# Optimization experiments

Hardware: AMD Instinct MI355X
Metric: run time of the kernel (lower is better)

Reference implementation:

```python
import jax, jax.numpy as jnp
import numpy as np

EPS = 1e-5

def _proj(x, W, g, b, m, v):
    # 1x1 conv (no bias) + BatchNorm2d (inference stats) + ReLU
    y = jnp.einsum('bchw,oc->bohw', x, W)
    scale = g / jnp.sqrt(v + EPS)
    y = y * scale[:, None, None] + (b - m * scale)[:, None, None]
    return jax.nn.relu(y)

def setup_inputs() -> dict:
    key = jax.random.key(0)
    B, C, H, W = 4, 192, 64, 64
    ks = jax.random.split(key, 10)
    d = {
        'lr_hsi': jax.random.normal(ks[0], (B, C, H, W), jnp.float32),
        'refine_hsi': jax.random.normal(ks[1], (B, C, H, W), jnp.float32),
    }
    for i, name in enumerate(['q', 'k', 'v', 't']):
        d['W' + name] = jax.random.normal(ks[2 + i], (C, C), jnp.float32) * 0.05
        d['g' + name] = jnp.ones((C,), jnp.float32)
        d['b' + name] = jnp.zeros((C,), jnp.float32)
        d['m' + name] = jnp.zeros((C,), jnp.float32)
        d['v' + name] = jnp.ones((C,), jnp.float32)
    return d

def reference(lr_hsi, refine_hsi,
              Wq, gq, bq, mq, vq,
              Wk, gk, bk, mk, vk,
              Wv, gv, bv, mv, vv,
              Wt, gt, bt, mt, vt):
    B, C, H, W = refine_hsi.shape
    HW = H * W
    q = _proj(refine_hsi, Wq, gq, bq, mq, vq).reshape(B, C, HW).transpose(0, 2, 1)  # [B, HWq, C]
    k = _proj(lr_hsi, Wk, gk, bk, mk, vk).reshape(B, C, HW)                          # [B, C, HWk]
    v = _proj(lr_hsi, Wv, gv, bv, mv, vv).reshape(B, C, HW).transpose(0, 2, 1)      # [B, HWk, C]
    corr = jnp.einsum('bqc,bck->bqk', q, k) * (C ** -0.5)  # [B, HWq, HWk]
    corr = jax.nn.softmax(corr, axis=1)  # NOTE: softmax over the QUERY axis (dim=1), as in source
    ss = jnp.einsum('bqk,bkc->bqc', corr, v)               # [B, HWq, C]
    ss = ss.transpose(0, 2, 1).reshape(B, C, H, W)
    out = _proj(ss, Wt, gt, bt, mt, vt)
    return (out, corr)
```

## Files before the change

### kernel.cpp

```cpp
#include <hip/hip_runtime.h>
#include <math.h>

typedef __attribute__((ext_vector_type(4))) float f32x4;
typedef __attribute__((ext_vector_type(8))) short bf16x8;

__device__ __forceinline__ unsigned short f2bf(float f) {
  unsigned int u = __builtin_bit_cast(unsigned int, f);
  u += 0x7FFFu + ((u >> 16) & 1u);
  return (unsigned short)(u >> 16);
}

__device__ __forceinline__ f32x4 mfma16(bf16x8 a, bf16x8 b, f32x4 c) {
  return __builtin_amdgcn_mfma_f32_16x16x32_bf16(a, b, c, 0, 0, 0);
}

__global__ void prep_kernel(const float* __restrict__ W, const float* __restrict__ g,
                            const float* __restrict__ bb, const float* __restrict__ mm,
                            const float* __restrict__ vv,
                            unsigned short* __restrict__ Wout, float* __restrict__ bout,
                            float alpha) {
  int idx = blockIdx.x * 256 + threadIdx.x;
  if (idx < 192 * 192) {
    int o = idx / 192;
    float s = g[o] * rsqrtf(vv[o] + 1e-5f);
    Wout[idx] = f2bf(W[idx] * s * alpha);
  }
  if (idx < 192) {
    float s = g[idx] * rsqrtf(vv[idx] + 1e-5f);
    bout[idx] = (bb[idx] - mm[idx] * s) * alpha;
  }
}

template <int LAYOUT>
__launch_bounds__(256)
__global__ void proj_kernel(const float* __restrict__ X,
                            const unsigned short* __restrict__ Wp,
                            const float* __restrict__ bias,
                            unsigned short* __restrict__ Yv) {
  const int o0 = blockIdx.x * 64;
  const int hw0 = blockIdx.y * 64;
  const int b = blockIdx.z;
  const int w = threadIdx.x >> 6, l = threadIdx.x & 63;
  const int l16 = l & 15, lg = l >> 4;
  const float* Xb = X + (size_t)b * 192 * 4096;

  f32x4 acc[4] = {f32x4{0,0,0,0}, f32x4{0,0,0,0}, f32x4{0,0,0,0}, f32x4{0,0,0,0}};

  for (int ks = 0; ks < 6; ++ks) {
    const int c0 = ks * 32 + lg * 8;
    bf16x8 a = *(const bf16x8*)(Wp + (size_t)(o0 + 16 * w + l16) * 192 + c0);
#pragma unroll
    for (int n = 0; n < 4; ++n) {
      const int hw = hw0 + 16 * n + l16;
      bf16x8 bfr;
#pragma unroll
      for (int j = 0; j < 8; ++j)
        bfr[j] = (short)f2bf(Xb[(size_t)(c0 + j) * 4096 + hw]);
      acc[n] = mfma16(a, bfr, acc[n]);
    }
  }

#pragma unroll
  for (int n = 0; n < 4; ++n) {
    const int hw = hw0 + 16 * n + l16;
    float vv4[4];
#pragma unroll
    for (int r = 0; r < 4; ++r) {
      const int o = o0 + 16 * w + lg * 4 + r;
      vv4[r] = fmaxf(acc[n][r] + bias[o], 0.0f);
    }
    if (LAYOUT == 1) {
      unsigned int lo = (unsigned)f2bf(vv4[0]) | ((unsigned)f2bf(vv4[1]) << 16);
      unsigned int hi = (unsigned)f2bf(vv4[2]) | ((unsigned)f2bf(vv4[3]) << 16);
      uint2 pk; pk.x = lo; pk.y = hi;
      *(uint2*)(Yv + ((size_t)b * 4096 + hw) * 192 + o0 + 16 * w + lg * 4) = pk;
    } else {
#pragma unroll
      for (int r = 0; r < 4; ++r) {
        const int o = o0 + 16 * w + lg * 4 + r;
        Yv[((size_t)b * 192 + o) * 4096 + hw] = f2bf(vv4[r]);
      }
    }
  }
}

template <int NS>
__launch_bounds__(256)
__global__ void proj_sum_kernel(const float* __restrict__ X,
                                const unsigned short* __restrict__ Wp,
                                const float* __restrict__ bias,
                                float* __restrict__ Yv) {
  const int o0 = blockIdx.x * 64;
  const int hw0 = blockIdx.y * 64;
  const int b = blockIdx.z;
  const int w = threadIdx.x >> 6, l = threadIdx.x & 63;
  const int l16 = l & 15, lg = l >> 4;
  const float* Xb = X + (size_t)b * 192 * 4096;
  const size_t sstride = (size_t)4 * 192 * 4096;

  f32x4 acc[4] = {f32x4{0,0,0,0}, f32x4{0,0,0,0}, f32x4{0,0,0,0}, f32x4{0,0,0,0}};

  for (int ks = 0; ks < 6; ++ks) {
    const int c0 = ks * 32 + lg * 8;
    bf16x8 a = *(const bf16x8*)(Wp + (size_t)(o0 + 16 * w + l16) * 192 + c0);
#pragma unroll
    for (int n = 0; n < 4; ++n) {
      const int hw = hw0 + 16 * n + l16;
      bf16x8 bfr;
#pragma unroll
      for (int j = 0; j < 8; ++j) {
        float s = Xb[(size_t)(c0 + j) * 4096 + hw];
#pragma unroll
        for (int ss = 1; ss < NS; ++ss)
          s += Xb[(size_t)(c0 + j) * 4096 + hw + ss * sstride];
        bfr[j] = (short)f2bf(s);
      }
      acc[n] = mfma16(a, bfr, acc[n]);
    }
  }

#pragma unroll
  for (int n = 0; n < 4; ++n) {
    const int hw = hw0 + 16 * n + l16;
#pragma unroll
    for (int r = 0; r < 4; ++r) {
      const int o = o0 + 16 * w + lg * 4 + r;
      Yv[((size_t)b * 192 + o) * 4096 + hw] = fmaxf(acc[n][r] + bias[o], 0.0f);
    }
  }
}

__launch_bounds__(256)
__global__ void pass1_kernel(const unsigned short* __restrict__ qp,
                             const unsigned short* __restrict__ kpT,
                             float* __restrict__ colsum) {
  const int q0 = blockIdx.x * 128, k0 = blockIdx.y * 128, b = blockIdx.z;
  const int w = threadIdx.x >> 6, l = threadIdx.x & 63;
  const int l16 = l & 15, lg = l >> 4;
  const unsigned short* qb = qp + (size_t)b * 4096 * 192;
  const unsigned short* kb = kpT + (size_t)b * 4096 * 192;

  __shared__ __align__(16) unsigned short kpl[128][200];
  __shared__ float cs[4][128];

  {
    const int t = threadIdx.x;
#pragma unroll
    for (int i = 0; i < 12; ++i) {
      int idx = t + i * 256;
      int row = idx / 24, cu = idx % 24;
      uint4 vdat = *(const uint4*)(kb + (size_t)(k0 + row) * 192 + cu * 8);
      *(uint4*)&kpl[row][cu * 8] = vdat;
    }
  }
  __syncthreads();

  f32x4 acc[2][8];
#pragma unroll
  for (int m = 0; m < 2; ++m)
#pragma unroll
    for (int n = 0; n < 8; ++n) acc[m][n] = f32x4{0, 0, 0, 0};

  for (int ks = 0; ks < 6; ++ks) {
    const int c0 = ks * 32 + lg * 8;
    bf16x8 a0 = *(const bf16x8*)(qb + (size_t)(q0 + 32 * w + l16) * 192 + c0);
    bf16x8 a1 = *(const bf16x8*)(qb + (size_t)(q0 + 32 * w + 16 + l16) * 192 + c0);
#pragma unroll
    for (int n = 0; n < 8; ++n) {
      bf16x8 bfr = *(const bf16x8*)&kpl[16 * n + l16][c0];
      acc[0][n] = mfma16(a0, bfr, acc[0][n]);
      acc[1][n] = mfma16(a1, bfr, acc[1][n]);
    }
  }

  float part[8];
#pragma unroll
  for (int n = 0; n < 8; ++n) {
    float s = 0.f;
#pragma unroll
    for (int r = 0; r < 4; ++r)
      s += __builtin_amdgcn_exp2f(acc[0][n][r]) + __builtin_amdgcn_exp2f(acc[1][n][r]);
    s += __shfl_xor(s, 16);
    s += __shfl_xor(s, 32);
    part[n] = s;
  }
  if (l < 16) {
#pragma unroll
    for (int n = 0; n < 8; ++n) cs[w][16 * n + l] = part[n];
  }
  __syncthreads();
  const int t = threadIdx.x;
  if (t < 128) {
    float s = cs[0][t] + cs[1][t] + cs[2][t] + cs[3][t];
    atomicAdd(&colsum[(size_t)b * 4096 + k0 + t], s);
  }
}

__global__ void invert_kernel(float* __restrict__ p, int n) {
  int i = blockIdx.x * 256 + threadIdx.x;
  if (i < n) p[i] = 1.0f / p[i];
}

template <int NS>
__launch_bounds__(512)
__global__ void pass2_kernel(const unsigned short* __restrict__ qp,
                             const unsigned short* __restrict__ kpT,
                             const unsigned short* __restrict__ vpN,
                             const float* __restrict__ rcol,
                             float* __restrict__ corr,
                             float* __restrict__ ssP) {
  const int q0 = blockIdx.x * 64;
  const int s = blockIdx.y;
  const int b = blockIdx.z;
  const int kc0 = s * (32 / NS);
  const int w = threadIdx.x >> 6, l = threadIdx.x & 63;
  const int l16 = l & 15, lg = l >> 4;
  const int mw = w & 1, nw = w >> 1;
  const unsigned short* qb = qp + (size_t)b * 4096 * 192;
  const unsigned short* kb = kpT + (size_t)b * 4096 * 192;
  const unsigned short* vb = vpN + (size_t)b * 192 * 4096;
  const float* rc = rcol + (size_t)b * 4096;
  float* corb = corr + (size_t)b * 4096 * 4096;
  float* ssb = ssP + (size_t)(s * 4 + b) * 192 * 4096;

  __shared__ __align__(16) float cor[64][132];

  bf16x8 af[2][6];
#pragma unroll
  for (int tm = 0; tm < 2; ++tm)
#pragma unroll
    for (int ks = 0; ks < 6; ++ks)
      af[tm][ks] = *(const bf16x8*)(qb + (size_t)(q0 + 16 * (2 * mw + tm) + l16) * 192 + ks * 32 + lg * 8);

  f32x4 ssa[2][3];
#pragma unroll
  for (int tm = 0; tm < 2; ++tm)
#pragma unroll
    for (int j = 0; j < 3; ++j) ssa[tm][j] = f32x4{0, 0, 0, 0};

  for (int kc = kc0; kc < kc0 + 32 / NS; ++kc) {
    const int k0 = kc * 128;
    f32x4 sa[2][2];
#pragma unroll
    for (int tm = 0; tm < 2; ++tm)
#pragma unroll
      for (int tn = 0; tn < 2; ++tn) sa[tm][tn] = f32x4{0, 0, 0, 0};

    for (int ks = 0; ks < 6; ++ks) {
      const int c0 = ks * 32 + lg * 8;
#pragma unroll
      for (int tn = 0; tn < 2; ++tn) {
        const int kcol = k0 + 16 * (2 * nw + tn) + l16;
        bf16x8 bfr = *(const bf16x8*)(kb + (size_t)kcol * 192 + c0);
        sa[0][tn] = mfma16(af[0][ks], bfr, sa[0][tn]);
        sa[1][tn] = mfma16(af[1][ks], bfr, sa[1][tn]);
      }
    }
    float rcv[2];
#pragma unroll
    for (int tn = 0; tn < 2; ++tn) rcv[tn] = rc[k0 + 16 * (2 * nw + tn) + l16];
#pragma unroll
    for (int tm = 0; tm < 2; ++tm)
#pragma unroll
      for (int tn = 0; tn < 2; ++tn)
#pragma unroll
        for (int r = 0; r < 4; ++r)
          sa[tm][tn][r] = __builtin_amdgcn_exp2f(sa[tm][tn][r]) * rcv[tn];

    __syncthreads();
#pragma unroll
    for (int tm = 0; tm < 2; ++tm)
#pragma unroll
      for (int tn = 0; tn < 2; ++tn) {
        const int col = 16 * (2 * nw + tn) + l16;
#pragma unroll
        for (int r = 0; r < 4; ++r)
          cor[16 * (2 * mw + tm) + lg * 4 + r][col] = sa[tm][tn][r];
      }
    __syncthreads();

    {
      const int t = threadIdx.x;
#pragma unroll
      for (int it = 0; it < 4; ++it) {
        int idx = t + it * 512;
        int row = idx >> 5, seg = idx & 31;
        f32x4 v4 = *(const f32x4*)&cor[row][seg * 4];
        __builtin_nontemporal_store(v4, (f32x4*)(corb + (size_t)(q0 + row) * 4096 + k0 + seg * 4));
      }
    }

#pragma unroll
    for (int ks2 = 0; ks2 < 4; ++ks2) {
      const int cc = ks2 * 32 + lg * 8;
      bf16x8 pa[2];
#pragma unroll
      for (int tm = 0; tm < 2; ++tm) {
        f32x4 p0 = *(const f32x4*)&cor[16 * (2 * mw + tm) + l16][cc];
        f32x4 p1 = *(const f32x4*)&cor[16 * (2 * mw + tm) + l16][cc + 4];
#pragma unroll
        for (int j = 0; j < 4; ++j) {
          pa[tm][j] = (short)f2bf(p0[j]);
          pa[tm][j + 4] = (short)f2bf(p1[j]);
        }
      }
#pragma unroll
      for (int j = 0; j < 3; ++j) {
        const int ccol = 16 * (nw + 4 * j) + l16;
        bf16x8 bfr = *(const bf16x8*)(vb + (size_t)ccol * 4096 + k0 + cc);
        ssa[0][j] = mfma16(pa[0], bfr, ssa[0][j]);
        ssa[1][j] = mfma16(pa[1], bfr, ssa[1][j]);
      }
    }
  }

#pragma unroll
  for (int tm = 0; tm < 2; ++tm)
#pragma unroll
    for (int j = 0; j < 3; ++j) {
      const int ccol = 16 * (nw + 4 * j) + l16;
#pragma unroll
      for (int r = 0; r < 4; ++r) {
        const int qrow = q0 + 16 * (2 * mw + tm) + lg * 4 + r;
        ssb[(size_t)ccol * 4096 + qrow] = ssa[tm][j][r];
      }
    }
}

extern "C" void kernel_launch(void* const* d_in, const int* in_sizes, int n_in,
                              void* d_out, int out_size, void* d_ws, size_t ws_size,
                              hipStream_t stream) {
  (void)in_sizes; (void)n_in; (void)out_size;
  const float* lr = (const float*)d_in[0];
  const float* refine = (const float*)d_in[1];

  char* ws = (char*)d_ws;
  unsigned short* w4 = (unsigned short*)(ws + 0);
  float* bias4 = (float*)(ws + 294912);
  unsigned short* qp = (unsigned short*)(ws + 297984);
  unsigned short* kp = (unsigned short*)(ws + 297984 + 6291456);
  unsigned short* vp = (unsigned short*)(ws + 297984 + 2 * 6291456);
  float* colsum = (float*)(ws + 297984 + 3 * 6291456);
  float* ssP = (float*)(ws + 297984 + 3 * 6291456 + 65536);

  const size_t base = 297984 + (size_t)3 * 6291456 + 65536;
  const size_t slab = (size_t)4 * 192 * 4096 * 4;
  int NS = (ws_size >= base + 2 * slab) ? 2 : 1;

  float* out0 = (float*)d_out;
  float* corr = out0 + 3145728;

  const float alpha = (float)(1.4426950408889634 / sqrt(192.0));

  for (int p = 0; p < 4; ++p) {
    prep_kernel<<<dim3(144), dim3(256), 0, stream>>>(
        (const float*)d_in[2 + 5 * p], (const float*)d_in[3 + 5 * p],
        (const float*)d_in[4 + 5 * p], (const float*)d_in[5 + 5 * p],
        (const float*)d_in[6 + 5 * p],
        w4 + p * 36864, bias4 + p * 192, p == 0 ? alpha : 1.0f);
  }
  hipMemsetAsync(colsum, 0, 65536, stream);

  proj_kernel<1><<<dim3(3, 64, 4), dim3(256), 0, stream>>>(refine, w4, bias4, qp);
  proj_kernel<1><<<dim3(3, 64, 4), dim3(256), 0, stream>>>(lr, w4 + 36864, bias4 + 192, kp);
  proj_kernel<0><<<dim3(3, 64, 4), dim3(256), 0, stream>>>(lr, w4 + 2 * 36864, bias4 + 2 * 192, vp);

  pass1_kernel<<<dim3(32, 32, 4), dim3(256), 0, stream>>>(qp, kp, colsum);
  invert_kernel<<<dim3(64), dim3(256), 0, stream>>>(colsum, 16384);

  if (NS == 2) {
    pass2_kernel<2><<<dim3(64, 2, 4), dim3(512), 0, stream>>>(qp, kp, vp, colsum, corr, ssP);
    proj_sum_kernel<2><<<dim3(3, 64, 4), dim3(256), 0, stream>>>(ssP, w4 + 3 * 36864, bias4 + 3 * 192, out0);
  } else {
    pass2_kernel<1><<<dim3(64, 1, 4), dim3(512), 0, stream>>>(qp, kp, vp, colsum, corr, ssP);
    proj_sum_kernel<1><<<dim3(3, 64, 4), dim3(256), 0, stream>>>(ssP, w4 + 3 * 36864, bias4 + 3 * 192, out0);
  }
}
```

Before: 293.8 us.

## Stage K tiles in swizzled double-buffered LDS and shrink key chunk to 64

The pass2 kernel now loads each 64-key K tile cooperatively into a double-buffered, XOR-swizzled shared-memory buffer. The next tile is prefetched into registers during the current tile's MFMAs and written to LDS afterwards, replacing the per-wave direct global loads of K fragments. The key chunk shrinks from 128 to 64 columns, with a matching smaller correlation staging buffer and adjusted store and PV loops. Launch bounds now request 4 blocks per CU, which constrains register use; the added LDS (about 65 KB per block) may itself limit occupancy.

```diff
diff --git a/kernel.cpp b/kernel.cpp
--- a/kernel.cpp
+++ b/kernel.cpp
@@ -202,7 +202,7 @@
 }
 
 template <int NS>
-__launch_bounds__(512)
+__launch_bounds__(512, 4)
 __global__ void pass2_kernel(const unsigned short* __restrict__ qp,
                              const unsigned short* __restrict__ kpT,
                              const unsigned short* __restrict__ vpN,
@@ -212,7 +212,8 @@
   const int q0 = blockIdx.x * 64;
   const int s = blockIdx.y;
   const int b = blockIdx.z;
-  const int kc0 = s * (32 / NS);
+  const int nchunk = 64 / NS;
+  const int kc0 = s * nchunk;
   const int w = threadIdx.x >> 6, l = threadIdx.x & 63;
   const int l16 = l & 15, lg = l >> 4;
   const int mw = w & 1, nw = w >> 1;
@@ -223,7 +224,11 @@
   float* corb = corr + (size_t)b * 4096 * 4096;
   float* ssb = ssP + (size_t)(s * 4 + b) * 192 * 4096;
 
-  __shared__ __align__(16) float cor[64][132];
+  __shared__ __align__(16) unsigned short kst[2][64 * 192];
+  __shared__ __align__(16) float cor[64][66];
+
+  const int u0 = threadIdx.x;
+  const int srow = u0 / 24 >= 64 ? 63 : u0 / 24;
 
   bf16x8 af[2][6];
 #pragma unroll
@@ -238,60 +243,83 @@
 #pragma unroll
     for (int j = 0; j < 3; ++j) ssa[tm][j] = f32x4{0, 0, 0, 0};
 
-  for (int kc = kc0; kc < kc0 + 32 / NS; ++kc) {
-    const int k0 = kc * 128;
-    f32x4 sa[2][2];
-#pragma unroll
-    for (int tm = 0; tm < 2; ++tm)
-#pragma unroll
-      for (int tn = 0; tn < 2; ++tn) sa[tm][tn] = f32x4{0, 0, 0, 0};
-
+  {
+    const int k0 = kc0 * 64;
+#pragma unroll
+    for (int i = 0; i < 3; ++i) {
+      int u = u0 + i * 512;
+      int row = u / 24, cu = u % 24;
+      uint4 vdat = *(const uint4*)(kb + (size_t)(k0 + row) * 192 + cu * 8);
+      *(uint4*)&kst[0][row * 192 + ((cu * 8) ^ ((row & 7) << 3))] = vdat;
+    }
+  }
+  __syncthreads();
+
+  const int krow = 16 * nw + l16;
+  const int kswz = (krow & 7) << 3;
+
+  for (int kc = kc0; kc < kc0 + nchunk; ++kc) {
+    const int k0 = kc * 64;
+    const int cur = (kc - kc0) & 1;
+    const bool havenext = (kc + 1 < kc0 + nchunk);
+
+    uint4 stg[3];
+    if (havenext) {
+      const int k0n = k0 + 64;
+#pragma unroll
+      for (int i = 0; i < 3; ++i) {
+        int u = u0 + i * 512;
+        int row = u / 24, cu = u % 24;
+        stg[i] = *(const uint4*)(kb + (size_t)(k0n + row) * 192 + cu * 8);
+      }
+    }
+
+    f32x4 sa[2];
+    sa[0] = f32x4{0, 0, 0, 0};
+    sa[1] = f32x4{0, 0, 0, 0};
     for (int ks = 0; ks < 6; ++ks) {
       const int c0 = ks * 32 + lg * 8;
-#pragma unroll
-      for (int tn = 0; tn < 2; ++tn) {
-        const int kcol = k0 + 16 * (2 * nw + tn) + l16;
-        bf16x8 bfr = *(const bf16x8*)(kb + (size_t)kcol * 192 + c0);
-        sa[0][tn] = mfma16(af[0][ks], bfr, sa[0][tn]);
-        sa[1][tn] = mfma16(af[1][ks], bfr, sa[1][tn]);
-      }
-    }
-    float rcv[2];
-#pragma unroll
-    for (int tn = 0; tn < 2; ++tn) rcv[tn] = rc[k0 + 16 * (2 * nw + tn) + l16];
+      bf16x8 kf = *(const bf16x8*)&kst[cur][krow * 192 + (c0 ^ kswz)];
+      sa[0] = mfma16(af[0][ks], kf, sa[0]);
+      sa[1] = mfma16(af[1][ks], kf, sa[1]);
+    }
+    const float rcv = rc[k0 + krow];
 #pragma unroll
     for (int tm = 0; tm < 2; ++tm)
 #pragma unroll
-      for (int tn = 0; tn < 2; ++tn)
-#pragma unroll
-        for (int r = 0; r < 4; ++r)
-          sa[tm][tn][r] = __builtin_amdgcn_exp2f(sa[tm][tn][r]) * rcv[tn];
+      for (int r = 0; r < 4; ++r)
+        sa[tm][r] = __builtin_amdgcn_exp2f(sa[tm][r]) * rcv;
 
     __syncthreads();
-#pragma unroll
-    for (int tm = 0; tm < 2; ++tm)
-#pragma unroll
-      for (int tn = 0; tn < 2; ++tn) {
-        const int col = 16 * (2 * nw + tn) + l16;
-#pragma unroll
-        for (int r = 0; r < 4; ++r)
-          cor[16 * (2 * mw + tm) + lg * 4 + r][col] = sa[tm][tn][r];
-      }
+
+#pragma unroll
+    for (int tm = 0; tm < 2; ++tm) {
+#pragma unroll
+      for (int r = 0; r < 4; ++r)
+        cor[16 * (2 * mw + tm) + lg * 4 + r][krow] = sa[tm][r];
+    }
+    if (havenext) {
+#pragma unroll
+      for (int i = 0; i < 3; ++i) {
+        int u = u0 + i * 512;
+        int row = u / 24, cu = u % 24;
+        *(uint4*)&kst[cur ^ 1][row * 192 + ((cu * 8) ^ ((row & 7) << 3))] = stg[i];
+      }
+    }
     __syncthreads();
 
     {
-      const int t = threadIdx.x;
-#pragma unroll
-      for (int it = 0; it < 4; ++it) {
-        int idx = t + it * 512;
-        int row = idx >> 5, seg = idx & 31;
+#pragma unroll
+      for (int it = 0; it < 2; ++it) {
+        int u = u0 + it * 512;
+        int row = u >> 4, seg = u & 15;
         f32x4 v4 = *(const f32x4*)&cor[row][seg * 4];
         __builtin_nontemporal_store(v4, (f32x4*)(corb + (size_t)(q0 + row) * 4096 + k0 + seg * 4));
       }
     }
 
 #pragma unroll
-    for (int ks2 = 0; ks2 < 4; ++ks2) {
+    for (int ks2 = 0; ks2 < 2; ++ks2) {
       const int cc = ks2 * 32 + lg * 8;
       bf16x8 pa[2];
 #pragma unroll
```

Measured after the change: 334.2 us. +13.7%, slower.

## Materialize bf16 exp matrix once, fold column normalization into V, split PV and corr

Applied to the files above, without the earlier changes.

Pass 1 now stores the exponentiated scores as a bf16 E buffer alongside the column sums, so the QK^T product is no longer recomputed in pass 2. The softmax normalization moves into V through a scaled-V kernel, PV becomes a plain bf16 GEMM over E, and a separate streaming kernel writes corr from E times the reciprocal column sums. The cost is a 128MB intermediate write and read, plus bf16 rounding of the exponentials before both corr and the PV product. The new path runs only when the workspace is large enough, otherwise the old recompute path is used.

```diff
diff --git a/kernel.cpp b/kernel.cpp
--- a/kernel.cpp
+++ b/kernel.cpp
@@ -8,6 +8,10 @@
   unsigned int u = __builtin_bit_cast(unsigned int, f);
   u += 0x7FFFu + ((u >> 16) & 1u);
   return (unsigned short)(u >> 16);
+}
+
+__device__ __forceinline__ float bf2f(unsigned short u) {
+  return __builtin_bit_cast(float, (unsigned int)u << 16);
 }
 
 __device__ __forceinline__ f32x4 mfma16(bf16x8 a, bf16x8 b, f32x4 c) {
@@ -131,15 +135,200 @@
 }
 
 __launch_bounds__(256)
-__global__ void pass1_kernel(const unsigned short* __restrict__ qp,
-                             const unsigned short* __restrict__ kpT,
-                             float* __restrict__ colsum) {
+__global__ void pass1_e_kernel(const unsigned short* __restrict__ qp,
+                               const unsigned short* __restrict__ kpT,
+                               unsigned short* __restrict__ E,
+                               float* __restrict__ colsum) {
   const int q0 = blockIdx.x * 128, k0 = blockIdx.y * 128, b = blockIdx.z;
   const int w = threadIdx.x >> 6, l = threadIdx.x & 63;
   const int l16 = l & 15, lg = l >> 4;
   const unsigned short* qb = qp + (size_t)b * 4096 * 192;
   const unsigned short* kb = kpT + (size_t)b * 4096 * 192;
 
+  __shared__ __align__(16) unsigned short smem[128 * 200];
+
+  {
+    const int t = threadIdx.x;
+#pragma unroll
+    for (int i = 0; i < 12; ++i) {
+      int idx = t + i * 256;
+      int row = idx / 24, cu = idx % 24;
+      uint4 vdat = *(const uint4*)(qb + (size_t)(q0 + row) * 192 + cu * 8);
+      *(uint4*)&smem[row * 200 + cu * 8] = vdat;
+    }
+  }
+  __syncthreads();
+
+  f32x4 acc[2][8];
+#pragma unroll
+  for (int m = 0; m < 2; ++m)
+#pragma unroll
+    for (int n = 0; n < 8; ++n) acc[m][n] = f32x4{0, 0, 0, 0};
+
+  for (int ks = 0; ks < 6; ++ks) {
+    const int c0 = ks * 32 + lg * 8;
+    bf16x8 a0 = *(const bf16x8*)(kb + (size_t)(k0 + 32 * w + l16) * 192 + c0);
+    bf16x8 a1 = *(const bf16x8*)(kb + (size_t)(k0 + 32 * w + 16 + l16) * 192 + c0);
+#pragma unroll
+    for (int n = 0; n < 8; ++n) {
+      bf16x8 bfr = *(const bf16x8*)&smem[(16 * n + l16) * 200 + c0];
+      acc[0][n] = mfma16(a0, bfr, acc[0][n]);
+      acc[1][n] = mfma16(a1, bfr, acc[1][n]);
+    }
+  }
+
+#pragma unroll
+  for (int m = 0; m < 2; ++m) {
+#pragma unroll
+    for (int r = 0; r < 4; ++r) {
+      float s = 0.f;
+#pragma unroll
+      for (int n = 0; n < 8; ++n) {
+        float e = __builtin_amdgcn_exp2f(acc[m][n][r]);
+        acc[m][n][r] = e;
+        s += e;
+      }
+      s += __shfl_xor(s, 1);
+      s += __shfl_xor(s, 2);
+      s += __shfl_xor(s, 4);
+      s += __shfl_xor(s, 8);
+      if (l16 == 0)
+        atomicAdd(&colsum[(size_t)b * 4096 + k0 + 32 * w + 16 * m + lg * 4 + r], s);
+    }
+  }
+
+  __syncthreads();
+#pragma unroll
+  for (int m = 0; m < 2; ++m)
+#pragma unroll
+    for (int n = 0; n < 8; ++n) {
+      unsigned int lo = (unsigned)f2bf(acc[m][n][0]) | ((unsigned)f2bf(acc[m][n][1]) << 16);
+      unsigned int hi = (unsigned)f2bf(acc[m][n][2]) | ((unsigned)f2bf(acc[m][n][3]) << 16);
+      uint2 pk; pk.x = lo; pk.y = hi;
+      *(uint2*)&smem[(16 * n + l16) * 144 + 32 * w + 16 * m + lg * 4] = pk;
+    }
+  __syncthreads();
+
+  {
+    const int t = threadIdx.x;
+#pragma unroll
+    for (int i = 0; i < 8; ++i) {
+      int idx = t + i * 256;
+      int row = idx >> 4, c16 = idx & 15;
+      uint4 vdat = *(const uint4*)&smem[row * 144 + c16 * 8];
+      *(uint4*)(E + (size_t)(b * 4096 + q0 + row) * 4096 + k0 + c16 * 8) = vdat;
+    }
+  }
+}
+
+__global__ void invert_kernel(float* __restrict__ p, int n) {
+  int i = blockIdx.x * 256 + threadIdx.x;
+  if (i < n) p[i] = 1.0f / p[i];
+}
+
+__launch_bounds__(256)
+__global__ void vscale_kernel(const unsigned short* __restrict__ vp,
+                              const float* __restrict__ rcol,
+                              unsigned short* __restrict__ vps) {
+  int i = blockIdx.x * 256 + threadIdx.x;
+  if (i >= 4 * 192 * 512) return;
+  int b = i / (192 * 512);
+  int k = (i & 511) * 8;
+  f32x4 rc0 = *(const f32x4*)(rcol + b * 4096 + k);
+  f32x4 rc1 = *(const f32x4*)(rcol + b * 4096 + k + 4);
+  bf16x8 v = *(const bf16x8*)(vp + (size_t)i * 8);
+  bf16x8 o;
+#pragma unroll
+  for (int j = 0; j < 4; ++j) {
+    o[j] = (short)f2bf(bf2f((unsigned short)v[j]) * rc0[j]);
+    o[j + 4] = (short)f2bf(bf2f((unsigned short)v[j + 4]) * rc1[j]);
+  }
+  *(bf16x8*)(vps + (size_t)i * 8) = o;
+}
+
+__launch_bounds__(256)
+__global__ void pv_kernel(const unsigned short* __restrict__ E,
+                          const unsigned short* __restrict__ vps,
+                          float* __restrict__ ssP) {
+  const int q0 = blockIdx.x * 64;
+  const int s = blockIdx.y;
+  const int b = blockIdx.z;
+  const int w = threadIdx.x >> 6, l = threadIdx.x & 63;
+  const int l16 = l & 15, lg = l >> 4;
+  const unsigned short* Eb = E + (size_t)b * 4096 * 4096;
+  const unsigned short* vb = vps + (size_t)b * 192 * 4096;
+  float* ssb = ssP + (size_t)(s * 4 + b) * 192 * 4096;
+
+  __shared__ __align__(16) unsigned short Est[64][88];
+
+  f32x4 ssa[12];
+#pragma unroll
+  for (int j = 0; j < 12; ++j) ssa[j] = f32x4{0, 0, 0, 0};
+
+  const int kc0 = s * 16;
+  for (int kc = kc0; kc < kc0 + 16; ++kc) {
+    const int k0 = kc * 64;
+    {
+      const int t = threadIdx.x;
+#pragma unroll
+      for (int i2 = 0; i2 < 2; ++i2) {
+        int idx = t + i2 * 256;
+        int row = idx >> 3, c8 = idx & 7;
+        uint4 vdat = *(const uint4*)(Eb + (size_t)(q0 + row) * 4096 + k0 + c8 * 8);
+        *(uint4*)&Est[row][c8 * 8] = vdat;
+      }
+    }
+    __syncthreads();
+#pragma unroll
+    for (int kstep = 0; kstep < 2; ++kstep) {
+      bf16x8 af = *(const bf16x8*)&Est[16 * w + l16][kstep * 32 + lg * 8];
+#pragma unroll
+      for (int j = 0; j < 12; ++j) {
+        bf16x8 bfr = *(const bf16x8*)(vb + (size_t)(16 * j + l16) * 4096 + k0 + kstep * 32 + lg * 8);
+        ssa[j] = mfma16(af, bfr, ssa[j]);
+      }
+    }
+    __syncthreads();
+  }
+
+#pragma unroll
+  for (int j = 0; j < 12; ++j)
+    *(f32x4*)(ssb + (size_t)(16 * j + l16) * 4096 + q0 + 16 * w + lg * 4) = ssa[j];
+}
+
+__launch_bounds__(256)
+__global__ void corr_kernel(const unsigned short* __restrict__ E,
+                            const float* __restrict__ rcol,
+                            float* __restrict__ corr) {
+  const size_t N = (size_t)4 * 4096 * 512;
+  for (size_t i = (size_t)blockIdx.x * 256 + threadIdx.x; i < N; i += (size_t)gridDim.x * 256) {
+    size_t bq = i >> 9;
+    int k = ((int)i & 511) * 8;
+    int b = (int)(bq >> 12);
+    bf16x8 e = *(const bf16x8*)(E + bq * 4096 + k);
+    f32x4 rc0 = *(const f32x4*)(rcol + b * 4096 + k);
+    f32x4 rc1 = *(const f32x4*)(rcol + b * 4096 + k + 4);
+    f32x4 o0, o1;
+#pragma unroll
+    for (int j = 0; j < 4; ++j) {
+      o0[j] = bf2f((unsigned short)e[j]) * rc0[j];
+      o1[j] = bf2f((unsigned short)e[j + 4]) * rc1[j];
+    }
+    __builtin_nontemporal_store(o0, (f32x4*)(corr + bq * 4096 + k));
+    __builtin_nontemporal_store(o1, (f32x4*)(corr + bq * 4096 + k + 4));
+  }
+}
+
+__launch_bounds__(256)
+__global__ void pass1_basic_kernel(const unsigned short* __restrict__ qp,
+                                   const unsigned short* __restrict__ kpT,
+                                   float* __restrict__ colsum) {
+  const int q0 = blockIdx.x * 128, k0 = blockIdx.y * 128, b = blockIdx.z;
+  const int w = threadIdx.x >> 6, l = threadIdx.x & 63;
+  const int l16 = l & 15, lg = l >> 4;
+  const unsigned short* qb = qp + (size_t)b * 4096 * 192;
+  const unsigned short* kb = kpT + (size_t)b * 4096 * 192;
+
   __shared__ __align__(16) unsigned short kpl[128][200];
   __shared__ float cs[4][128];
 
@@ -196,19 +385,14 @@
   }
 }
 
-__global__ void invert_kernel(float* __restrict__ p, int n) {
-  int i = blockIdx.x * 256 + threadIdx.x;
-  if (i < n) p[i] = 1.0f / p[i];
-}
-
 template <int NS>
 __launch_bounds__(512)
-__global__ void pass2_kernel(const unsigned short* __restrict__ qp,
-                             const unsigned short* __restrict__ kpT,
-                             const unsigned short* __restrict__ vpN,
-                             const float* __restrict__ rcol,
-                             float* __restrict__ corr,
-                             float* __restrict__ ssP) {
+__global__ void pass2_basic_kernel(const unsigned short* __restrict__ qp,
+                                   const unsigned short* __restrict__ kpT,
+                                   const unsigned short* __restrict__ vpN,
+                                   const float* __restrict__ rcol,
+                                   float* __restrict__ corr,
+                                   float* __restrict__ ssP) {
   const int q0 = blockIdx.x * 64;
   const int s = blockIdx.y;
   const int b = blockIdx.z;
@@ -340,12 +524,11 @@
   unsigned short* qp = (unsigned short*)(ws + 297984);
   unsigned short* kp = (unsigned short*)(ws + 297984 + 6291456);
   unsigned short* vp = (unsigned short*)(ws + 297984 + 2 * 6291456);
-  float* colsum = (float*)(ws + 297984 + 3 * 6291456);
-  float* ssP = (float*)(ws + 297984 + 3 * 6291456 + 65536);
-
-  const size_t base = 297984 + (size_t)3 * 6291456 + 65536;
-  const size_t slab = (size_t)4 * 192 * 4096 * 4;
-  int NS = (ws_size >= base + 2 * slab) ? 2 : 1;
+  float* colsum = (float*)(ws + 19172352);
+  unsigned short* vps = (unsigned short*)(ws + 19237888);
+  float* ssP = (float*)(ws + 25529344);
+  unsigned short* Ebuf = (unsigned short*)(ws + 75860992);
+  const size_t NEW_NEED = 210078720;
 
   float* out0 = (float*)d_out;
   float* corr = out0 + 3145728;
@@ -365,14 +548,17 @@
   proj_kernel<1><<<dim3(3, 64, 4), dim3(256), 0, stream>>>(lr, w4 + 36864, bias4 + 192, kp);
   proj_kernel<0><<<dim3(3, 64, 4), dim3(256), 0, stream>>>(lr, w4 + 2 * 36864, bias4 + 2 * 192, vp);
 
-  pass1_kernel<<<dim3(32, 32, 4), dim3(256), 0, stream>>>(qp, kp, colsum);
-  invert_kernel<<<dim3(64), dim3(256), 0, stream>>>(colsum, 16384);
-
-  if (NS == 2) {
-    pass2_kernel<2><<<dim3(64, 2, 4), dim3(512), 0, stream>>>(qp, kp, vp, colsum, corr, ssP);
+  if (ws_size >= NEW_NEED) {
+    pass1_e_kernel<<<dim3(32, 32, 4), dim3(256), 0, stream>>>(qp, kp, Ebuf, colsum);
+    invert_kernel<<<dim3(64), dim3(256), 0, stream>>>(colsum, 16384);
+    vscale_kernel<<<dim3(1536), dim3(256), 0, stream>>>(vp, colsum, vps);
+    pv_kernel<<<dim3(64, 4, 4), dim3(256), 0, stream>>>(Ebuf, vps, ssP);
+    proj_sum_kernel<4><<<dim3(3, 64, 4), dim3(256), 0, stream>>>(ssP, w4 + 3 * 36864, bias4 + 3 * 192, out0);
+    corr_kernel<<<dim3(2048), dim3(256), 0, stream>>>(Ebuf, colsum, corr);
+  } else {
+    pass1_basic_kernel<<<dim3(32, 32, 4), dim3(256), 0, stream>>>(qp, kp, colsum);
+    invert_kernel<<<dim3(64), dim3(256), 0, stream>>>(colsum, 16384);
+    pass2_basic_kernel<2><<<dim3(64, 2, 4), dim3(512), 0, stream>>>(qp, kp, vp, colsum, corr, ssP);
     proj_sum_kernel<2><<<dim3(3, 64, 4), dim3(256), 0, stream>>>(ssP, w4 + 3 * 36864, bias4 + 3 * 192, out0);
-  } else {
-    pass2_kernel<1><<<dim3(64, 1, 4), dim3(512), 0, stream>>>(qp, kp, vp, colsum, corr, ssP);
-    proj_sum_kernel<1><<<dim3(3, 64, 4), dim3(256), 0, stream>>>(ssP, w4 + 3 * 36864, bias4 + 3 * 192, out0);
-  }
-}
+  }
+}
```

New measurement: 430.3 us. 1.46x slower.
